# Kernel tuning notes

Hardware: AMD Instinct MI355X
Metric: run time of the kernel (lower is better)

Reference implementation:

```python
import jax, jax.numpy as jnp
import numpy as np

B, S, H, NH = 4, 2048, 1024, 16
D = H // NH  # head_dim = 64


def setup_inputs() -> dict:
    key = jax.random.key(0)
    ks = jax.random.split(key, 8)
    hidden_states = jax.random.normal(ks[0], (B, S, H), dtype=jnp.float32)
    attention_mask = jnp.zeros((B, 1, 1, S), dtype=jnp.float32)  # additive, bidirectional
    # RoPE tables (cos/sin per position, full head_dim)
    inv_freq = 1.0 / (10000.0 ** (jnp.arange(0, D, 2, dtype=jnp.float32) / D))
    t = jnp.arange(S, dtype=jnp.float32)
    freqs = jnp.outer(t, inv_freq)              # [S, D/2]
    emb = jnp.concatenate([freqs, freqs], -1)   # [S, D]
    cos, sin = jnp.cos(emb), jnp.sin(emb)
    scale = 1.0 / np.sqrt(H)
    Wq = jax.random.normal(ks[1], (H, H), dtype=jnp.float32) * scale
    Wk = jax.random.normal(ks[2], (H, H), dtype=jnp.float32) * scale
    Wv = jax.random.normal(ks[3], (H, H), dtype=jnp.float32) * scale
    Wo = jax.random.normal(ks[4], (H, H), dtype=jnp.float32) * scale
    return {"hidden_states": hidden_states, "attention_mask": attention_mask,
            "cos": cos, "sin": sin, "Wq": Wq, "Wk": Wk, "Wv": Wv, "Wo": Wo}


def _rotate_half(x):
    x1, x2 = jnp.split(x, 2, axis=-1)
    return jnp.concatenate([-x2, x1], axis=-1)


def _rope(x, cos, sin):
    # x: [B, NH, S, D]; cos/sin: [S, D]
    c = cos[None, None, :, :]
    s = sin[None, None, :, :]
    return x * c + _rotate_half(x) * s


def reference(hidden_states, attention_mask, cos, sin, Wq, Wk, Wv, Wo):
    b, s, h = hidden_states.shape
    # QKV projections (torch Linear: x @ W^T)
    def proj(W):
        y = jnp.einsum('bsh,oh->bso', hidden_states, W)
        return y.reshape(b, s, NH, D).transpose(0, 2, 1, 3)  # [B, NH, S, D]
    q, k, v = proj(Wq), proj(Wk), proj(Wv)
    q = _rope(q, cos, sin)
    k = _rope(k, cos, sin)
    scale = D ** -0.5
    scores = jnp.einsum('bhqd,bhkd->bhqk', q, k) * scale + attention_mask
    attn = jax.nn.softmax(scores, axis=-1)
    out = jnp.einsum('bhqk,bhkd->bhqd', attn, v)            # [B, NH, S, D]
    out = out.transpose(0, 2, 1, 3).reshape(b, s, h)        # [B, S, H]
    return jnp.einsum('bsh,oh->bso', out, Wo)
```

## Files before the change

kernel.cpp:

```cpp
#include <hip/hip_runtime.h>


typedef __bf16 bf16x8 __attribute__((ext_vector_type(8)));
typedef float f32x4 __attribute__((ext_vector_type(4)));
typedef float f32x16 __attribute__((ext_vector_type(16)));
typedef unsigned short u16x8 __attribute__((ext_vector_type(8)));
typedef unsigned short u16x4 __attribute__((ext_vector_type(4)));
typedef const __attribute__((address_space(1))) void* gptr_t;
typedef __attribute__((address_space(3))) void* lptr_t;

template <int N> struct ic { static constexpr int v = N; };

__device__ __forceinline__ unsigned short f2bf(float f) {
  union { float f; unsigned u; } v; v.f = f;
  unsigned r = (v.u + 0x7fffu + ((v.u >> 16) & 1u)) >> 16;
  return (unsigned short)r;
}

__device__ __forceinline__ unsigned short f2bfn(float f) {
  union { __bf16 h; unsigned short u; } v;
  v.h = (__bf16)f;
  return v.u;
}

__device__ __forceinline__ unsigned cvtpk(float lo, float hi_) {
  unsigned r;
  asm("v_cvt_pk_bf16_f32 %0, %1, %2" : "=v"(r) : "v"(lo), "v"(hi_));
  return r;
}

__device__ __forceinline__ void gld16(const void* g, void* l) {
  __builtin_amdgcn_global_load_lds((gptr_t)g, (lptr_t)l, 16, 0, 0);
}

__global__ __launch_bounds__(256) void cvt_all(
    const float* __restrict__ hidden, const float* __restrict__ Wq,
    const float* __restrict__ Wk, const float* __restrict__ Wv,
    const float* __restrict__ Wo, unsigned short* __restrict__ Xb,
    unsigned short* __restrict__ Wb) {
  size_t i8 = ((size_t)blockIdx.x * 256 + threadIdx.x) * 8;
  const float* src;
  unsigned short* dst;
  if (i8 < 8388608) {
    src = hidden + i8;
    dst = Xb + i8;
  } else {
    size_t r = i8 - 8388608;
    int wsel = (int)(r >> 20);
    size_t off = r & 1048575;
    const float* wsrc = (wsel == 0) ? Wq : (wsel == 1) ? Wk : (wsel == 2) ? Wv : Wo;
    src = wsrc + off;
    dst = Wb + r;
  }
  f32x4 a = *(const f32x4*)(src);
  f32x4 b = *(const f32x4*)(src + 4);
  u16x8 o;
  o[0] = f2bf(a[0]); o[1] = f2bf(a[1]); o[2] = f2bf(a[2]); o[3] = f2bf(a[3]);
  o[4] = f2bf(b[0]); o[5] = f2bf(b[1]); o[6] = f2bf(b[2]); o[7] = f2bf(b[3]);
  *(u16x8*)dst = o;
}

__global__ __launch_bounds__(768, 3) void gemm_qkv(
    const unsigned short* __restrict__ A,
    const unsigned short* __restrict__ W0, const unsigned short* __restrict__ W1,
    const unsigned short* __restrict__ W2,
    const float* __restrict__ cosT, const float* __restrict__ sinT,
    unsigned short* __restrict__ Qh, unsigned short* __restrict__ Kh,
    unsigned short* __restrict__ Vh) {
  __shared__ char sm[131072];
  const int tid = threadIdx.x, lane = tid & 63, w = tid >> 6;
  const int l15 = lane & 15, h2 = lane >> 4;
  const int z = w >> 2, sub = w & 3;
  const int wm = sub >> 1, wn = sub & 1;
  const int wg = blockIdx.x;
  const int work = (wg & 7) * 64 + (wg >> 3);
  const int bx = work & 7, by = work >> 3;
  const int brow = by * 128;
  const int bcol = bx * 128;

  const char* Abase = (const char*)A + (size_t)brow * 2048;
  const char* Wb0 = (const char*)W0 + (size_t)bcol * 2048;
  const char* Wb1 = (const char*)W1 + (size_t)bcol * 2048;
  const char* Wb2 = (const char*)W2 + (size_t)bcol * 2048;

  const char* gsrc[6];
  int gdst[6];
#pragma unroll
  for (int i = 0; i < 6; ++i) {
    int g = tid + i * 768;
    bool val = g < 4096;
    int gg = val ? g : 0;
    int r = (gg & 1023) >> 3;
    int sw = ((gg & 7) * 16) ^ ((r & 7) << 4);
    const char* base;
    if (gg < 1024) base = Abase;
    else {
      int zz = (gg >> 10) - 1;
      base = (zz == 0) ? Wb0 : (zz == 1 ? Wb1 : Wb2);
    }
    gsrc[i] = val ? (base + (size_t)r * 2048 + sw) : nullptr;
    gdst[i] = gg * 16;
  }

  f32x4 acc[4][4];
#pragma unroll
  for (int m = 0; m < 4; ++m)
#pragma unroll
    for (int n = 0; n < 4; ++n) acc[m][n] = (f32x4){0.f, 0.f, 0.f, 0.f};

#pragma unroll
  for (int i = 0; i < 6; ++i)
    if (gsrc[i]) gld16(gsrc[i], sm + gdst[i]);

  for (int kt = 0; kt < 16; ++kt) {
    const int cur = kt & 1, nxt = cur ^ 1;
    if (kt < 15) {
#pragma unroll
      for (int i = 0; i < 6; ++i)
        if (gsrc[i]) gld16(gsrc[i] + (kt + 1) * 128, sm + nxt * 65536 + gdst[i]);
      if (w < 4) asm volatile("s_waitcnt vmcnt(6)" ::: "memory");
      else       asm volatile("s_waitcnt vmcnt(5)" ::: "memory");
    } else {
      asm volatile("s_waitcnt vmcnt(0)" ::: "memory");
    }
    __builtin_amdgcn_sched_barrier(0);
    __builtin_amdgcn_s_barrier();
    __builtin_amdgcn_sched_barrier(0);

    const char* Asw = sm + cur * 65536;
    const char* Bsw = sm + cur * 65536 + 16384 + z * 16384;
#pragma unroll
    for (int kk = 0; kk < 2; ++kk) {
      int kb = kk * 64 + h2 * 16;
      bf16x8 af[4], bfr[4];
#pragma unroll
      for (int m = 0; m < 4; ++m) {
        int r = wm * 64 + m * 16 + l15;
        af[m] = *(const bf16x8*)(Asw + r * 128 + (kb ^ ((r & 7) << 4)));
      }
#pragma unroll
      for (int n = 0; n < 4; ++n) {
        int r = wn * 64 + n * 16 + l15;
        bfr[n] = *(const bf16x8*)(Bsw + r * 128 + (kb ^ ((r & 7) << 4)));
      }
#pragma unroll
      for (int m = 0; m < 4; ++m)
#pragma unroll
        for (int n = 0; n < 4; ++n)
          acc[m][n] = __builtin_amdgcn_mfma_f32_16x16x32_bf16(af[m], bfr[n],
                                                              acc[m][n], 0, 0, 0);
    }
    __builtin_amdgcn_sched_barrier(0);
    __builtin_amdgcn_s_barrier();
  }

  const int h = bx * 2 + wn;
  if (z == 2) {
#pragma unroll
    for (int m = 0; m < 4; ++m) {
      int row0 = brow + wm * 64 + m * 16 + h2 * 4;
      int b = row0 >> 11, s0 = row0 & 2047;
      size_t base = (size_t)(b * 16 + h) * 64 * 2048 + s0;
#pragma unroll
      for (int n = 0; n < 4; ++n) {
        int dl = n * 16 + l15;
        u16x4 pw;
#pragma unroll
        for (int i = 0; i < 4; ++i) pw[i] = f2bf(acc[m][n][i]);
        *(u16x4*)(Vh + base + (size_t)dl * 2048) = pw;
      }
    }
  } else {
    unsigned short* dst = (z == 0) ? Qh : Kh;
    const float qs = (z == 0) ? 0.18033688f : 1.0f;
#pragma unroll
    for (int m = 0; m < 4; ++m)
#pragma unroll
      for (int i = 0; i < 4; ++i) {
        int row = brow + wm * 64 + m * 16 + h2 * 4 + i;
        int b = row >> 11, s = row & 2047;
        size_t hb2 = ((size_t)(b * 16 + h) * 2048 + s) * 64;
#pragma unroll
        for (int n = 0; n < 2; ++n) {
          int dl = n * 16 + l15;
          float c = cosT[s * 64 + dl], sn = sinT[s * 64 + dl];
          float lo = acc[m][n][i], hi = acc[m][n + 2][i];
          dst[hb2 + dl] = f2bf((lo * c - hi * sn) * qs);
          dst[hb2 + dl + 32] = f2bf((hi * c + lo * sn) * qs);
        }
      }
  }
}

__global__ __launch_bounds__(256, 3) void gemm_k(
    const unsigned short* __restrict__ A, const unsigned short* __restrict__ W0,
    float* __restrict__ Cout) {
  __shared__ char sm[32768];
  char* As = sm;
  char* Bs = sm + 16384;
  const int tid = threadIdx.x, lane = tid & 63, w = tid >> 6;
  const int wm = w >> 1, wn = w & 1;
  const int brow = blockIdx.y * 128;
  const int bcol = blockIdx.x * 128;

  f32x4 acc[4][4];
#pragma unroll
  for (int m = 0; m < 4; ++m)
#pragma unroll
    for (int n = 0; n < 4; ++n) acc[m][n] = (f32x4){0.f, 0.f, 0.f, 0.f};

  const char* Abase = (const char*)A + (size_t)brow * 2048;
  const char* Bbase = (const char*)W0 + (size_t)bcol * 2048;

  for (int kt = 0; kt < 1024; kt += 64) {
#pragma unroll
    for (int c = 0; c < 4; ++c) {
      int Lb = w * 4096 + c * 1024;
      int L = Lb + lane * 16;
      int r = L >> 7, kb = L & 127;
      int sw = kb ^ ((r & 7) << 4);
      gld16(Abase + (size_t)r * 2048 + kt * 2 + sw, As + Lb);
      gld16(Bbase + (size_t)r * 2048 + kt * 2 + sw, Bs + Lb);
    }
    __syncthreads();
#pragma unroll
    for (int kk = 0; kk < 2; ++kk) {
      int kb = kk * 64 + (lane >> 4) * 16;
      bf16x8 af[4], bfr[4];
#pragma unroll
      for (int m = 0; m < 4; ++m) {
        int r = wm * 64 + m * 16 + (lane & 15);
        af[m] = *(const bf16x8*)(As + r * 128 + (kb ^ ((r & 7) << 4)));
      }
#pragma unroll
      for (int n = 0; n < 4; ++n) {
        int r = wn * 64 + n * 16 + (lane & 15);
        bfr[n] = *(const bf16x8*)(Bs + r * 128 + (kb ^ ((r & 7) << 4)));
      }
#pragma unroll
      for (int m = 0; m < 4; ++m)
#pragma unroll
        for (int n = 0; n < 4; ++n)
          acc[m][n] = __builtin_amdgcn_mfma_f32_16x16x32_bf16(af[m], bfr[n],
                                                              acc[m][n], 0, 0, 0);
    }
    __syncthreads();
  }

#pragma unroll
  for (int m = 0; m < 4; ++m)
#pragma unroll
    for (int n = 0; n < 4; ++n)
#pragma unroll
      for (int i = 0; i < 4; ++i) {
        int row = brow + wm * 64 + m * 16 + (lane >> 4) * 4 + i;
        int col = bcol + wn * 64 + n * 16 + (lane & 15);
        Cout[(size_t)row * 1024 + col] = acc[m][n][i];
      }
}

__global__ __launch_bounds__(256, 4) void attn_k(
    const unsigned short* __restrict__ Q, const unsigned short* __restrict__ K,
    const unsigned short* __restrict__ Vt, const float* __restrict__ mask,
    unsigned short* __restrict__ O) {
  __shared__ char Ks[2][8192];
  __shared__ char Vs[2][8192];
  __shared__ float l_arr[4][32];
  const int tid = threadIdx.x, lane = tid & 63, w = tid >> 6;
  const int q31 = lane & 31, hi = lane >> 5;
  const int wg = blockIdx.x;
  const int work = (wg & 7) * 128 + (wg >> 3);
  const int qt = work & 15, hl = work >> 4;
  const int h = hl & 15, b = hl >> 4;
  const size_t hb = (size_t)(b * 16 + h) * (2048 * 64);
  const int q0 = qt * 128 + w * 32;
  const float L2E = 1.44269504f;
  const float MREF = 12.0f;
  const int rdo = q31 * 32 + hi * 16;

  bf16x8 qb[4];
  {
    const char* qrow = (const char*)(Q + hb + (size_t)(q0 + q31) * 64);
#pragma unroll
    for (int ks = 0; ks < 4; ++ks)
      qb[ks] = *(const bf16x8*)(qrow + ks * 32 + hi * 16);
  }

  float l_part = 0.f;
  f32x16 oacc[2];
#pragma unroll
  for (int e = 0; e < 16; ++e) { oacc[0][e] = 0.f; oacc[1][e] = 0.f; }

  int koff0, koff1, vof0, vof1;
  {
    int L0 = w * 2048 + lane * 16;
    int c0 = L0 >> 12, ks0 = (L0 >> 10) & 3, q0l = (L0 >> 5) & 31,
        hi0 = (L0 >> 4) & 1;
    int row0 = c0 * 32 + q0l, kb0 = ks0 * 32 + hi0 * 16;
    koff0 = row0 * 128 + kb0;
    vof0 = row0 * 4096 + kb0;
    int L1 = L0 + 1024;
    int c1 = L1 >> 12, ks1 = (L1 >> 10) & 3, q1l = (L1 >> 5) & 31,
        hi1 = (L1 >> 4) & 1;
    int row1 = c1 * 32 + q1l, kb1 = ks1 * 32 + hi1 * 16;
    koff1 = row1 * 128 + kb1;
    vof1 = row1 * 4096 + kb1;
  }
  const char* Kg = (const char*)(K + hb);
  const char* Vg = (const char*)(Vt + hb);
  const float* mp = mask + (size_t)b * 2048;

  gld16(Kg + koff0, Ks[0] + w * 2048);
  gld16(Kg + koff1, Ks[0] + w * 2048 + 1024);
  gld16(Vg + vof0, Vs[0] + w * 2048);
  gld16(Vg + vof1, Vs[0] + w * 2048 + 1024);

  auto body = [&](auto curc, int t) {
    constexpr int cur = decltype(curc)::v;
    constexpr int nxt = 1 - cur;
    if (t < 31) {
      const char* kp = Kg + (size_t)(t + 1) * 8192;
      const char* vp = Vg + (size_t)(t + 1) * 128;
      gld16(kp + koff0, Ks[nxt] + w * 2048);
      gld16(kp + koff1, Ks[nxt] + w * 2048 + 1024);
      gld16(vp + vof0, Vs[nxt] + w * 2048);
      gld16(vp + vof1, Vs[nxt] + w * 2048 + 1024);
      asm volatile("s_waitcnt vmcnt(4)" ::: "memory");
    } else {
      asm volatile("s_waitcnt vmcnt(0)" ::: "memory");
    }
    __builtin_amdgcn_sched_barrier(0);
    __builtin_amdgcn_s_barrier();
    __builtin_amdgcn_sched_barrier(0);

    const float* mrow = mp + t * 64;

    f32x16 sacc[2];
#pragma unroll
    for (int c = 0; c < 2; ++c) {
#pragma unroll
      for (int g = 0; g < 4; ++g) {
        f32x4 mv = *(const f32x4*)(mrow + c * 32 + g * 8 + hi * 4);
#pragma unroll
        for (int i = 0; i < 4; ++i)
          sacc[c][g * 4 + i] = fmaf(mv[i], L2E, -MREF);
      }
      __builtin_amdgcn_s_setprio(1);
#pragma unroll
      for (int ks = 0; ks < 4; ++ks) {
        bf16x8 kf =
            *(const bf16x8*)(Ks[cur] + (c * 4 + ks) * 1024 + rdo);
        sacc[c] = __builtin_amdgcn_mfma_f32_32x32x16_bf16(kf, qb[ks], sacc[c],
                                                          0, 0, 0);
      }
      __builtin_amdgcn_s_setprio(0);
#pragma unroll
      for (int e = 0; e < 16; ++e)
        sacc[c][e] = __builtin_amdgcn_exp2f(sacc[c][e]);
      float s0 = (sacc[c][0] + sacc[c][1]) + (sacc[c][2] + sacc[c][3]);
      float s1 = (sacc[c][4] + sacc[c][5]) + (sacc[c][6] + sacc[c][7]);
      float s2 = (sacc[c][8] + sacc[c][9]) + (sacc[c][10] + sacc[c][11]);
      float s3 = (sacc[c][12] + sacc[c][13]) + (sacc[c][14] + sacc[c][15]);
      l_part += (s0 + s1) + (s2 + s3);
    }

    __builtin_amdgcn_s_setprio(1);
#pragma unroll
    for (int c = 0; c < 2; ++c) {
#pragma unroll
      for (int par = 0; par < 2; ++par) {
        const int t2 = c * 2 + par;
        unsigned a0 = cvtpk(sacc[c][par * 8 + 0], sacc[c][par * 8 + 1]);
        unsigned a1 = cvtpk(sacc[c][par * 8 + 2], sacc[c][par * 8 + 3]);
        unsigned b0 = cvtpk(sacc[c][par * 8 + 4], sacc[c][par * 8 + 5]);
        unsigned b1 = cvtpk(sacc[c][par * 8 + 6], sacc[c][par * 8 + 7]);
        asm("v_permlane32_swap_b32 %0, %1" : "+v"(a0), "+v"(b0));
        asm("v_permlane32_swap_b32 %0, %1" : "+v"(a1), "+v"(b1));
        union { unsigned u[4]; bf16x8 v; } pu;
        pu.u[0] = a0; pu.u[1] = a1; pu.u[2] = b0; pu.u[3] = b1;
        bf16x8 vf0 = *(const bf16x8*)(Vs[cur] + t2 * 1024 + rdo);
        bf16x8 vf1 = *(const bf16x8*)(Vs[cur] + 4096 + t2 * 1024 + rdo);
        oacc[0] = __builtin_amdgcn_mfma_f32_32x32x16_bf16(pu.v, vf0, oacc[0],
                                                          0, 0, 0);
        oacc[1] = __builtin_amdgcn_mfma_f32_32x32x16_bf16(pu.v, vf1, oacc[1],
                                                          0, 0, 0);
      }
    }
    __builtin_amdgcn_s_setprio(0);
    __builtin_amdgcn_sched_barrier(0);
    __builtin_amdgcn_s_barrier();
  };

  for (int t = 0; t < 32; t += 2) {
    body(ic<0>{}, t);
    body(ic<1>{}, t + 1);
  }

  float lr = l_part + __shfl_xor(l_part, 32, 64);
  l_arr[w][q31] = 1.0f / lr;

#pragma unroll
  for (int g = 0; g < 4; ++g) {
    f32x4 iv = *(const f32x4*)(&l_arr[w][g * 8 + hi * 4]);
    const int qrow = q0 + g * 8 + hi * 4;
#pragma unroll
    for (int i = 0; i < 4; ++i) {
      size_t rb = (size_t)(b * 2048 + qrow + i) * 1024 + h * 64;
      O[rb + q31] = f2bfn(oacc[0][g * 4 + i] * iv[i]);
      O[rb + 32 + q31] = f2bfn(oacc[1][g * 4 + i] * iv[i]);
    }
  }
}

extern "C" void kernel_launch(void* const* d_in, const int* in_sizes, int n_in,
                              void* d_out, int out_size, void* d_ws, size_t ws_size,
                              hipStream_t stream) {
  const float* hidden = (const float*)d_in[0];
  const float* amask = (const float*)d_in[1];
  const float* cosT = (const float*)d_in[2];
  const float* sinT = (const float*)d_in[3];
  const float* Wq = (const float*)d_in[4];
  const float* Wk = (const float*)d_in[5];
  const float* Wv = (const float*)d_in[6];
  const float* Wo = (const float*)d_in[7];
  float* out = (float*)d_out;

  if (ws_size < (size_t)92274688) return;
  unsigned short* Xb = (unsigned short*)d_ws;
  unsigned short* Wqb = Xb + (size_t)8192 * 1024;
  unsigned short* Wkb = Wqb + (size_t)1024 * 1024;
  unsigned short* Wvb = Wkb + (size_t)1024 * 1024;
  unsigned short* Wob = Wvb + (size_t)1024 * 1024;
  unsigned short* Qh = Wob + (size_t)1024 * 1024;
  unsigned short* Kh = Qh + (size_t)8388608;
  unsigned short* Vt = Kh + (size_t)8388608;
  unsigned short* Ob = Vt + (size_t)8388608;

  cvt_all<<<6144, 256, 0, stream>>>(hidden, Wq, Wk, Wv, Wo, Xb, Wqb);

  gemm_qkv<<<512, 768, 0, stream>>>(Xb, Wqb, Wkb, Wvb, cosT, sinT, Qh, Kh, Vt);
  attn_k<<<1024, 256, 0, stream>>>(Qh, Kh, Vt, amask, Ob);
  gemm_k<<<dim3(8, 64), 256, 0, stream>>>(Ob, Wob, out);
}
```

Measured before the change: 192.4 us.

## Double-buffer LDS loads in output GEMM and remap blocks for locality

The output projection GEMM now double-buffers its shared memory tiles: it prefetches the next K-tile with direct global-to-LDS loads while computing on the current one, using partial vmcnt waits and raw barriers. The 2D grid becomes a 1D grid with a remap of block index to tile, so that consecutive blocks spread across column tiles and neighbouring work shares A rows. The LDS footprint doubles and launch bounds drop to 2 blocks per CU, trading occupancy for overlap of memory and compute.

```diff
diff --git a/kernel.cpp b/kernel.cpp
--- a/kernel.cpp
+++ b/kernel.cpp
@@ -192,16 +192,17 @@
   }
 }
 
-__global__ __launch_bounds__(256, 3) void gemm_k(
+__global__ __launch_bounds__(256, 2) void gemm_k(
     const unsigned short* __restrict__ A, const unsigned short* __restrict__ W0,
     float* __restrict__ Cout) {
-  __shared__ char sm[32768];
-  char* As = sm;
-  char* Bs = sm + 16384;
+  __shared__ char sm[65536];
   const int tid = threadIdx.x, lane = tid & 63, w = tid >> 6;
   const int wm = w >> 1, wn = w & 1;
-  const int brow = blockIdx.y * 128;
-  const int bcol = blockIdx.x * 128;
+  const int wg = blockIdx.x;
+  const int work = (wg & 7) * 64 + (wg >> 3);
+  const int bx = work & 7, by = work >> 3;
+  const int brow = by * 128;
+  const int bcol = bx * 128;
 
   f32x4 acc[4][4];
 #pragma unroll
@@ -212,17 +213,44 @@
   const char* Abase = (const char*)A + (size_t)brow * 2048;
   const char* Bbase = (const char*)W0 + (size_t)bcol * 2048;
 
-  for (int kt = 0; kt < 1024; kt += 64) {
-#pragma unroll
-    for (int c = 0; c < 4; ++c) {
-      int Lb = w * 4096 + c * 1024;
-      int L = Lb + lane * 16;
-      int r = L >> 7, kb = L & 127;
-      int sw = kb ^ ((r & 7) << 4);
-      gld16(Abase + (size_t)r * 2048 + kt * 2 + sw, As + Lb);
-      gld16(Bbase + (size_t)r * 2048 + kt * 2 + sw, Bs + Lb);
-    }
-    __syncthreads();
+  const char* srcA[4];
+  const char* srcB[4];
+  int dstO[4];
+#pragma unroll
+  for (int c = 0; c < 4; ++c) {
+    int Lb = w * 4096 + c * 1024;
+    int L = Lb + lane * 16;
+    int r = L >> 7, kb = L & 127;
+    int sw = kb ^ ((r & 7) << 4);
+    srcA[c] = Abase + (size_t)r * 2048 + sw;
+    srcB[c] = Bbase + (size_t)r * 2048 + sw;
+    dstO[c] = Lb;
+  }
+
+#pragma unroll
+  for (int c = 0; c < 4; ++c) {
+    gld16(srcA[c], sm + dstO[c]);
+    gld16(srcB[c], sm + 16384 + dstO[c]);
+  }
+
+  for (int kt = 0; kt < 16; ++kt) {
+    const int cur = kt & 1, nxt = cur ^ 1;
+    if (kt < 15) {
+#pragma unroll
+      for (int c = 0; c < 4; ++c) {
+        gld16(srcA[c] + (kt + 1) * 128, sm + nxt * 32768 + dstO[c]);
+        gld16(srcB[c] + (kt + 1) * 128, sm + nxt * 32768 + 16384 + dstO[c]);
+      }
+      asm volatile("s_waitcnt vmcnt(8)" ::: "memory");
+    } else {
+      asm volatile("s_waitcnt vmcnt(0)" ::: "memory");
+    }
+    __builtin_amdgcn_sched_barrier(0);
+    __builtin_amdgcn_s_barrier();
+    __builtin_amdgcn_sched_barrier(0);
+
+    const char* As = sm + cur * 32768;
+    const char* Bs = sm + cur * 32768 + 16384;
 #pragma unroll
     for (int kk = 0; kk < 2; ++kk) {
       int kb = kk * 64 + (lane >> 4) * 16;
@@ -244,7 +272,8 @@
           acc[m][n] = __builtin_amdgcn_mfma_f32_16x16x32_bf16(af[m], bfr[n],
                                                               acc[m][n], 0, 0, 0);
     }
-    __syncthreads();
+    __builtin_amdgcn_sched_barrier(0);
+    __builtin_amdgcn_s_barrier();
   }
 
 #pragma unroll
@@ -440,5 +469,5 @@
 
   gemm_qkv<<<512, 768, 0, stream>>>(Xb, Wqb, Wkb, Wvb, cosT, sinT, Qh, Kh, Vt);
   attn_k<<<1024, 256, 0, stream>>>(Qh, Kh, Vt, amask, Ob);
-  gemm_k<<<dim3(8, 64), 256, 0, stream>>>(Ob, Wob, out);
-}
+  gemm_k<<<512, 256, 0, stream>>>(Ob, Wob, out);
+}
```

Result: no change. 191.6 us, median of 3 (-0.5%).
